# Kernel tuning notes

Hardware: AMD Instinct MI355X
Metric: run time of the kernel (lower is better)

## Reference

```python
import jax, jax.numpy as jnp
import numpy as np

TAU = 0.5
EPS = 1e-12  # F.normalize eps


def _l2_normalize(z):
    n = jnp.linalg.norm(z, axis=1, keepdims=True)
    return z / jnp.maximum(n, EPS)


def _semi_loss(a, b):
    # a, b: [N, d], already raw embeddings; normalize then exp(sim/tau)
    an = _l2_normalize(a)
    bn = _l2_normalize(b)
    refl = jnp.exp(jnp.matmul(an, an.T) / TAU)      # [N, N]
    between = jnp.exp(jnp.matmul(an, bn.T) / TAU)   # [N, N]
    pos = jnp.diagonal(between)
    denom = refl.sum(axis=1) + between.sum(axis=1) - jnp.diagonal(refl)
    return -jnp.log(pos / denom)


def setup_inputs() -> dict:
    key = jax.random.key(0)
    k1, k2 = jax.random.split(key)
    z1 = jax.random.normal(k1, (8192, 256), dtype=jnp.float32)
    z2 = jax.random.normal(k2, (8192, 256), dtype=jnp.float32)
    return {"z1": z1, "z2": z2, "mean": 1}


def reference(z1, z2, mean):
    l1 = _semi_loss(z1, z2)
    l2 = _semi_loss(z2, z1)
    ret = (l1 + l2) * 0.5
    return ret.mean() if mean else ret.sum()
```

## Files before the change

### kernel.cpp

```cpp
#include <hip/hip_runtime.h>
#include <hip/hip_bf16.h>
#include <hip/hip_fp8.h>

#define N_ROWS 8192
#define NZ 16384
#define DIM 256
#define TAU_INV 2.0f
#define BT 128
#define AT 64
#define NTILE 128
#define NCHUNK 16
#define SEGT 4
#define NSEG 4224
#define PSTRIDE 768

typedef float f32x4 __attribute__((ext_vector_type(4)));
typedef long lx2 __attribute__((ext_vector_type(2)));

__global__ __launch_bounds__(256) void normalize_kernel(
    const float* __restrict__ z1, const float* __restrict__ z2,
    unsigned char* __restrict__ Z8, float* __restrict__ pos)
{
    const int tid = threadIdx.x;
    const int wave = tid >> 6;
    const int lane = tid & 63;
    const int row = blockIdx.x * 4 + wave;

    const float4 a = ((const float4*)(z1 + (size_t)row * DIM))[lane];
    const float4 b = ((const float4*)(z2 + (size_t)row * DIM))[lane];

    auto wsum = [&](float v) -> float {
        #pragma unroll
        for (int m = 1; m < 64; m <<= 1) v += __shfl_xor(v, m, 64);
        return v;
    };

    const float na2 = wsum(a.x*a.x + a.y*a.y + a.z*a.z + a.w*a.w);
    const float nb2 = wsum(b.x*b.x + b.y*b.y + b.z*b.z + b.w*b.w);
    const float sa = 16.0f / sqrtf(na2);
    const float sb = 16.0f / sqrtf(nb2);

    const float av[4] = {a.x*sa, a.y*sa, a.z*sa, a.w*sa};
    const float bv[4] = {b.x*sb, b.y*sb, b.z*sb, b.w*sb};
    unsigned char pa[4], pb[4];
    float qd = 0.0f;
    #pragma unroll
    for (int k = 0; k < 4; ++k) {
        __hip_fp8_e4m3 qa(av[k]);
        __hip_fp8_e4m3 qb(bv[k]);
        pa[k] = qa.__x; pb[k] = qb.__x;
        qd += float(qa) * float(qb);
    }
    const int g  = (lane >> 1) & 7;
    const int pp = ((g & 3) << 1) | (g >> 2);
    const int off = (lane >> 4) * 64 + pp * 8 + (lane & 1) * 4;
    *(uchar4*)(Z8 + (size_t)row * DIM + off) = *(uchar4*)pa;
    *(uchar4*)(Z8 + (size_t)(N_ROWS + row) * DIM + off) = *(uchar4*)pb;

    qd = wsum(qd);
    if (lane == 0) pos[row] = qd * 0.00390625f;
}

#define MFMA8(A, B, C) __builtin_amdgcn_mfma_f32_16x16x32_fp8_fp8(A, B, C, 0, 0, 0)

#define STAGE(TF, KH, SL)                                                      \
  { const unsigned char* gsrc = pb0 + (size_t)(TF) * 32768 + (KH) * 128;       \
    _Pragma("unroll")                                                          \
    for (int c = 0; c < 4; ++c)                                                \
      __builtin_amdgcn_global_load_lds(                                        \
        (const __attribute__((address_space(1))) void*)(gsrc + c * 2048),      \
        (__attribute__((address_space(3))) void*)(Ls + wvLds + (SL)*4096 + c*1024), \
        16, 0, 0); }

#define MFMA_HALF(KH)                                                          \
  __builtin_amdgcn_s_setprio(1);                                               \
  _Pragma("unroll")                                                            \
  for (int fr = 0; fr < 4; ++fr) {                                             \
    acc[fr][0] = MFMA8(aR[KH][0][fr].x, b00.x, acc[fr][0]);                    \
    acc[fr][0] = MFMA8(aR[KH][0][fr].y, b00.y, acc[fr][0]);                    \
    acc[fr][1] = MFMA8(aR[KH][0][fr].x, b10.x, acc[fr][1]);                    \
    acc[fr][1] = MFMA8(aR[KH][0][fr].y, b10.y, acc[fr][1]);                    \
  }                                                                            \
  _Pragma("unroll")                                                            \
  for (int fr = 0; fr < 4; ++fr) {                                             \
    acc[fr][0] = MFMA8(aR[KH][1][fr].x, b01.x, acc[fr][0]);                    \
    acc[fr][0] = MFMA8(aR[KH][1][fr].y, b01.y, acc[fr][0]);                    \
    acc[fr][1] = MFMA8(aR[KH][1][fr].x, b11.x, acc[fr][1]);                    \
    acc[fr][1] = MFMA8(aR[KH][1][fr].y, b11.y, acc[fr][1]);                    \
  }

#define PHASE(KH, SLOT, NW, DOISS, TF2, KH2, SLOT2)                            \
  {                                                                            \
    if (DOISS) STAGE(TF2, KH2, SLOT2);                                         \
    asm volatile("s_waitcnt vmcnt(" #NW ")" ::: "memory");                     \
    lx2 b00, b10, b01, b11;                                                    \
    asm volatile("ds_read_b128 %0, %1" : "=v"(b00) : "v"(bA00 + (SLOT)*4096)); \
    asm volatile("ds_read_b128 %0, %1" : "=v"(b10) : "v"(bA10 + (SLOT)*4096)); \
    asm volatile("ds_read_b128 %0, %1" : "=v"(b01) : "v"(bA01 + (SLOT)*4096)); \
    asm volatile("ds_read_b128 %0, %1" : "=v"(b11) : "v"(bA11 + (SLOT)*4096)); \
    asm volatile("s_waitcnt lgkmcnt(0)" ::: "memory");                         \
    __builtin_amdgcn_sched_barrier(0);                                         \
    MFMA_HALF(KH)                                                              \
    __builtin_amdgcn_s_setprio(0);                                             \
  }

#define EPILOG(T)                                                              \
  if ((T) < nt) {                                                              \
    _Pragma("unroll")                                                          \
    for (int fr = 0; fr < 4; ++fr)                                             \
      _Pragma("unroll")                                                        \
      for (int fc = 0; fc < 2; ++fc)                                           \
        _Pragma("unroll")                                                      \
        for (int r = 0; r < 4; ++r)                                            \
          acc[fr][fc][r] = exp2f(acc[fr][fc][r] * SC);                         \
    if ((T) == 0 && s4 == 0) {                                                 \
      const int add = (ri & 1) << 6;                                           \
      _Pragma("unroll")                                                        \
      for (int fr = 0; fr < 4; ++fr) {                                         \
        const int gi = fr * 16 + lq * 4;                                       \
        _Pragma("unroll")                                                      \
        for (int fc = 0; fc < 2; ++fc) {                                       \
          const int cj = wv * 32 + fc * 16 + lm;                               \
          _Pragma("unroll")                                                    \
          for (int r = 0; r < 4; ++r)                                          \
            if (cj <= gi + r + add) acc[fr][fc][r] = 0.0f;                     \
        }                                                                      \
      }                                                                        \
    }                                                                          \
    _Pragma("unroll")                                                          \
    for (int fr = 0; fr < 4; ++fr)                                             \
      _Pragma("unroll")                                                        \
      for (int r = 0; r < 4; ++r)                                              \
        rowacc[fr][r] += acc[fr][0][r] + acc[fr][1][r];                        \
    _Pragma("unroll")                                                          \
    for (int fc = 0; fc < 2; ++fc) {                                           \
      float s_ = 0.0f;                                                         \
      _Pragma("unroll")                                                        \
      for (int fr = 0; fr < 4; ++fr)                                           \
        _Pragma("unroll")                                                      \
        for (int r = 0; r < 4; ++r) s_ += acc[fr][fc][r];                      \
      colacc[T][fc] = s_;                                                      \
    }                                                                          \
  }

template <bool TWO_STAGE>
__global__ __launch_bounds__(256, 3) void gram_kernel(
    const unsigned char* __restrict__ Z,
    float* __restrict__ part, float* __restrict__ S)
{
    const int sid = (blockIdx.x & 7) * (NSEG / 8) + (blockIdx.x >> 3);
    int g = (int)((260.0f - sqrtf(67600.0f - 16.0f * (float)sid)) * 0.125f);
    g = g < 0 ? 0 : (g > 31 ? 31 : g);
    while (260 * g - 4 * g * g > sid) --g;
    while (g < 31 && 260 * (g + 1) - 4 * (g + 1) * (g + 1) <= sid) ++g;
    const int local = sid - (260 * g - 4 * g * g);
    const int v  = 32 - g;
    const int r8i = local / v;
    const int s4 = local - r8i * v;
    const int ri = 8 * g + r8i;
    const int tj0 = (ri >> 1) + SEGT * s4;
    const int nt = (NTILE - tj0 < SEGT) ? (NTILE - tj0) : SEGT;
    const int tf1 = nt > 1 ? 1 : 0;
    const int tf2 = nt > 2 ? 2 : tf1;
    const int tf3 = nt > 3 ? 3 : tf2;

    __shared__ unsigned char Ls[49152];

    const int tid  = threadIdx.x;
    const int wv   = tid >> 6;
    const int lane = tid & 63;
    const int lm = lane & 15, lq = lane >> 4;
    const unsigned wvLds = wv * 12288;

    lx2 aR[2][2][4];
    {
        const unsigned char* pa = Z + (size_t)(ri * AT + lm) * DIM + lq * 16;
        #pragma unroll
        for (int fr = 0; fr < 4; ++fr)
            #pragma unroll
            for (int kh = 0; kh < 2; ++kh)
                #pragma unroll
                for (int s = 0; s < 2; ++s)
                    aR[kh][s][fr] =
                        *(const lx2*)(pa + fr * 4096 + kh * 128 + s * 64);
    }

    const int l8 = lane >> 3;
    const int g7 = lane & 7;
    const unsigned char* pb0 =
        Z + (size_t)(tj0 * BT + wv * 32 + l8) * DIM + ((g7 ^ l8) << 4);

    const unsigned ldsBase = (unsigned)(unsigned long long)
        (__attribute__((address_space(3))) unsigned char*)Ls;
    const unsigned wvB = ldsBase + wvLds + (unsigned)(lm * 128);
    const unsigned q0 = (unsigned)(((lq    ) ^ (lm & 7)) << 4);
    const unsigned q1 = (unsigned)(((lq + 4) ^ (lm & 7)) << 4);
    const unsigned bA00 = wvB + q0;
    const unsigned bA01 = wvB + q1;
    const unsigned bA10 = wvB + 2048 + q0;
    const unsigned bA11 = wvB + 2048 + q1;

    const float SC = 2.8853900817779268f / 256.0f;

    f32x4 rowacc[4] = {};
    float colacc[4][2] = {};

    STAGE(0, 0, 0)
    STAGE(0, 1, 1)

    { f32x4 acc[4][2] = {};
      PHASE(0, 0, 8, 1, tf1, 0, 2)
      PHASE(1, 1, 8, 1, tf1, 1, 0)
      EPILOG(0)
    }
    { f32x4 acc[4][2] = {};
      PHASE(0, 2, 8, 1, tf2, 0, 1)
      PHASE(1, 0, 8, 1, tf2, 1, 2)
      EPILOG(1)
    }
    { f32x4 acc[4][2] = {};
      PHASE(0, 1, 8, 1, tf3, 0, 0)
      PHASE(1, 2, 8, 1, tf3, 1, 1)
      EPILOG(2)
    }
    { f32x4 acc[4][2] = {};
      PHASE(0, 0, 4, 0, 0, 0, 0)
      PHASE(1, 1, 0, 0, 0, 0, 0)
      EPILOG(3)
    }

    #pragma unroll
    for (int t = 0; t < 4; ++t)
        #pragma unroll
        for (int fc = 0; fc < 2; ++fc) {
            float s = colacc[t][fc];
            s += __shfl_xor(s, 16, 64);
            s += __shfl_xor(s, 32, 64);
            if (lq == 0) {
                const int cj = wv * 32 + fc * 16 + lm;
                if (TWO_STAGE)
                    part[(size_t)sid * PSTRIDE + 256 + t * 128 + cj] = s;
                else if (t < nt)
                    atomicAdd(&S[(tj0 + t) * BT + cj], s);
            }
        }

    float* dstr = TWO_STAGE ? (part + (size_t)sid * PSTRIDE) : nullptr;
    #pragma unroll
    for (int fr = 0; fr < 4; ++fr) {
        f32x4 rs;
        #pragma unroll
        for (int r = 0; r < 4; ++r) {
            float s = rowacc[fr][r];
            s += __shfl_xor(s, 1, 64);
            s += __shfl_xor(s, 2, 64);
            s += __shfl_xor(s, 4, 64);
            s += __shfl_xor(s, 8, 64);
            rs[r] = s;
        }
        if (lm == 0) {
            const int rr = fr * 16 + lq * 4;
            if (TWO_STAGE) *(f32x4*)(dstr + wv * 64 + rr) = rs;
            else {
                #pragma unroll
                for (int r = 0; r < 4; ++r)
                    atomicAdd(&S[ri * AT + rr + r], rs[r]);
            }
        }
    }
}

__global__ __launch_bounds__(256) void reduce_kernel(
    const float* __restrict__ part, float* __restrict__ S2,
    float* __restrict__ out)
{
    const int chunk = blockIdx.y;
    const int tid = threadIdx.x;
    const int r = blockIdx.x * 256 + tid;
    const int ri = r >> 6, rr = r & 63;
    const int gg = ri >> 3;
    const int nseg = 32 - gg;
    const int sid0 = 260 * gg - 4 * gg * gg + (ri & 7) * nseg;
    const int tj = r >> 7, cc = r & 127;
    const int nr = 2 * tj + 2;
    const int T = 4 * nseg + nr;

    if (chunk == 0 && r == 0) out[0] = 0.0f;

    float s = 0.0f;
    for (int m = chunk; m < T; m += NCHUNK) {
        size_t addr;
        if (m < 4 * nseg) {
            addr = (size_t)(sid0 + (m >> 2)) * PSTRIDE + (m & 3) * 64 + rr;
        } else {
            const int rip = m - 4 * nseg;
            const int dtj = tj - (rip >> 1);
            const int gp = rip >> 3;
            const int sidc = 260 * gp - 4 * gp * gp + (rip & 7) * (32 - gp)
                           + (dtj >> 2);
            addr = (size_t)sidc * PSTRIDE + 256 + (dtj & 3) * 128 + cc;
        }
        s += part[addr];
    }
    S2[(size_t)chunk * NZ + r] = s;
}

__global__ __launch_bounds__(256) void loss2_kernel(
    const float* __restrict__ S2, const float* __restrict__ pos,
    float* __restrict__ out)
{
    const int i = blockIdx.x * 256 + threadIdx.x;
    float den1 = 0.0f, den2 = 0.0f;
    #pragma unroll
    for (int c = 0; c < NCHUNK; ++c) {
        den1 += S2[(size_t)c * NZ + i];
        den2 += S2[(size_t)c * NZ + N_ROWS + i];
    }
    float v = 0.5f * (logf(den1) + logf(den2)) - TAU_INV * pos[i];

    __shared__ float red[4];
    #pragma unroll
    for (int m = 1; m < 64; m <<= 1) v += __shfl_xor(v, m, 64);
    if ((threadIdx.x & 63) == 0) red[threadIdx.x >> 6] = v;
    __syncthreads();
    if (threadIdx.x == 0)
        atomicAdd(out, (red[0] + red[1] + red[2] + red[3]) * (1.0f / N_ROWS));
}

__global__ __launch_bounds__(256) void loss_kernel(
    const float* __restrict__ S, const float* __restrict__ pos,
    float* __restrict__ out)
{
    const int i = blockIdx.x * 256 + threadIdx.x;
    float v = 0.5f * (logf(S[i]) + logf(S[N_ROWS + i])) - TAU_INV * pos[i];

    __shared__ float red[4];
    #pragma unroll
    for (int m = 1; m < 64; m <<= 1) v += __shfl_xor(v, m, 64);
    if ((threadIdx.x & 63) == 0) red[threadIdx.x >> 6] = v;
    __syncthreads();
    if (threadIdx.x == 0)
        atomicAdd(out, (red[0] + red[1] + red[2] + red[3]) * (1.0f / N_ROWS));
}

extern "C" void kernel_launch(void* const* d_in, const int* in_sizes, int n_in,
                              void* d_out, int out_size, void* d_ws, size_t ws_size,
                              hipStream_t stream)
{
    const float* z1 = (const float*)d_in[0];
    const float* z2 = (const float*)d_in[1];
    float* out = (float*)d_out;

    char* ws = (char*)d_ws;
    unsigned char* Z8 = (unsigned char*)ws;
    float* pos  = (float*)(ws + 4194304);
    float* S2   = (float*)(ws + 4227072);
    float* part = (float*)(ws + 5275648);
    const size_t need = 5275648 + (size_t)NSEG * PSTRIDE * 4;

    normalize_kernel<<<N_ROWS / 4, 256, 0, stream>>>(z1, z2, Z8, pos);

    if (ws_size >= need) {
        gram_kernel<true><<<NSEG, 256, 0, stream>>>(Z8, part, nullptr);
        dim3 rg(NZ / 256, NCHUNK);
        reduce_kernel<<<rg, 256, 0, stream>>>(part, S2, out);
        loss2_kernel<<<N_ROWS / 256, 256, 0, stream>>>(S2, pos, out);
    } else {
        hipMemsetAsync(S2, 0, NZ * sizeof(float), stream);
        hipMemsetAsync(out, 0, sizeof(float), stream);
        gram_kernel<false><<<NSEG, 256, 0, stream>>>(Z8, nullptr, S2);
        loss_kernel<<<N_ROWS / 256, 256, 0, stream>>>(S2, pos, out);
    }
}
```

Before: 160.6 us.

## Share B tiles across waves via common LDS with 2x2 wave grid

Replaces the per-wave private B staging (each wave loading its own 32 columns) with a shared LDS buffer that all four waves fill cooperatively, and reorganizes the 64x128 tile so waves form a 2x2 grid (32 rows x 64 columns each). Each wave now holds fewer A fragments in registers and reads four B fragments per k-step. Block barriers are added before each phase, and the partial-sum layout and reduction indexing are updated to handle the extra row/column partials. The change aims at better operand reuse and fewer registers, at the cost of block-wide synchronization and larger partial buffers.

```diff
diff --git a/kernel.cpp b/kernel.cpp
--- a/kernel.cpp
+++ b/kernel.cpp
@@ -12,7 +12,7 @@
 #define NCHUNK 16
 #define SEGT 4
 #define NSEG 4224
-#define PSTRIDE 768
+#define PSTRIDE 1152
 
 typedef float f32x4 __attribute__((ext_vector_type(4)));
 typedef long lx2 __attribute__((ext_vector_type(2)));
@@ -64,63 +64,73 @@
 #define MFMA8(A, B, C) __builtin_amdgcn_mfma_f32_16x16x32_fp8_fp8(A, B, C, 0, 0, 0)
 
 #define STAGE(TF, KH, SL)                                                      \
-  { const unsigned char* gsrc = pb0 + (size_t)(TF) * 32768 + (KH) * 128;       \
+  { const unsigned char* gsrc = pbSt + (size_t)(TF) * 32768 + (KH) * 128;      \
     _Pragma("unroll")                                                          \
     for (int c = 0; c < 4; ++c)                                                \
       __builtin_amdgcn_global_load_lds(                                        \
         (const __attribute__((address_space(1))) void*)(gsrc + c * 2048),      \
-        (__attribute__((address_space(3))) void*)(Ls + wvLds + (SL)*4096 + c*1024), \
+        (__attribute__((address_space(3))) void*)(Ls + (SL) * 16384 + (wv * 4 + c) * 1024), \
         16, 0, 0); }
 
-#define MFMA_HALF(KH)                                                          \
-  __builtin_amdgcn_s_setprio(1);                                               \
-  _Pragma("unroll")                                                            \
-  for (int fr = 0; fr < 4; ++fr) {                                             \
-    acc[fr][0] = MFMA8(aR[KH][0][fr].x, b00.x, acc[fr][0]);                    \
-    acc[fr][0] = MFMA8(aR[KH][0][fr].y, b00.y, acc[fr][0]);                    \
-    acc[fr][1] = MFMA8(aR[KH][0][fr].x, b10.x, acc[fr][1]);                    \
-    acc[fr][1] = MFMA8(aR[KH][0][fr].y, b10.y, acc[fr][1]);                    \
-  }                                                                            \
-  _Pragma("unroll")                                                            \
-  for (int fr = 0; fr < 4; ++fr) {                                             \
-    acc[fr][0] = MFMA8(aR[KH][1][fr].x, b01.x, acc[fr][0]);                    \
-    acc[fr][0] = MFMA8(aR[KH][1][fr].y, b01.y, acc[fr][0]);                    \
-    acc[fr][1] = MFMA8(aR[KH][1][fr].x, b11.x, acc[fr][1]);                    \
-    acc[fr][1] = MFMA8(aR[KH][1][fr].y, b11.y, acc[fr][1]);                    \
-  }
-
-#define PHASE(KH, SLOT, NW, DOISS, TF2, KH2, SLOT2)                            \
+#define DSR(DST, ADDR, SOFF)                                                   \
+  asm volatile("ds_read_b128 %0, %1 offset:" SOFF : "=v"(DST) : "v"(ADDR));
+
+#define PHASE(KH, SOFF, VMW, DOST, TF2, KH2, SL2)                              \
   {                                                                            \
-    if (DOISS) STAGE(TF2, KH2, SLOT2);                                         \
-    asm volatile("s_waitcnt vmcnt(" #NW ")" ::: "memory");                     \
-    lx2 b00, b10, b01, b11;                                                    \
-    asm volatile("ds_read_b128 %0, %1" : "=v"(b00) : "v"(bA00 + (SLOT)*4096)); \
-    asm volatile("ds_read_b128 %0, %1" : "=v"(b10) : "v"(bA10 + (SLOT)*4096)); \
-    asm volatile("ds_read_b128 %0, %1" : "=v"(b01) : "v"(bA01 + (SLOT)*4096)); \
-    asm volatile("ds_read_b128 %0, %1" : "=v"(b11) : "v"(bA11 + (SLOT)*4096)); \
+    asm volatile("s_waitcnt vmcnt(" VMW ") lgkmcnt(0)\n\ts_barrier" ::: "memory"); \
+    if (DOST) STAGE(TF2, KH2, SL2)                                             \
+    lx2 b00, b01, b02, b03, b10, b11, b12, b13;                                \
+    DSR(b00, bR0, SOFF) DSR(b01, bR1, SOFF)                                    \
+    DSR(b02, bR2, SOFF) DSR(b03, bR3, SOFF)                                    \
+    DSR(b10, bS0, SOFF) DSR(b11, bS1, SOFF)                                    \
+    DSR(b12, bS2, SOFF) DSR(b13, bS3, SOFF)                                    \
+    asm volatile("s_waitcnt lgkmcnt(4)" ::: "memory");                         \
+    __builtin_amdgcn_sched_barrier(0);                                         \
+    __builtin_amdgcn_s_setprio(1);                                             \
+    _Pragma("unroll")                                                          \
+    for (int fr = 0; fr < 2; ++fr) {                                           \
+      acc[fr][0] = MFMA8(aR[KH][0][fr].x, b00.x, acc[fr][0]);                  \
+      acc[fr][0] = MFMA8(aR[KH][0][fr].y, b00.y, acc[fr][0]);                  \
+      acc[fr][1] = MFMA8(aR[KH][0][fr].x, b01.x, acc[fr][1]);                  \
+      acc[fr][1] = MFMA8(aR[KH][0][fr].y, b01.y, acc[fr][1]);                  \
+      acc[fr][2] = MFMA8(aR[KH][0][fr].x, b02.x, acc[fr][2]);                  \
+      acc[fr][2] = MFMA8(aR[KH][0][fr].y, b02.y, acc[fr][2]);                  \
+      acc[fr][3] = MFMA8(aR[KH][0][fr].x, b03.x, acc[fr][3]);                  \
+      acc[fr][3] = MFMA8(aR[KH][0][fr].y, b03.y, acc[fr][3]);                  \
+    }                                                                          \
     asm volatile("s_waitcnt lgkmcnt(0)" ::: "memory");                         \
     __builtin_amdgcn_sched_barrier(0);                                         \
-    MFMA_HALF(KH)                                                              \
+    _Pragma("unroll")                                                          \
+    for (int fr = 0; fr < 2; ++fr) {                                           \
+      acc[fr][0] = MFMA8(aR[KH][1][fr].x, b10.x, acc[fr][0]);                  \
+      acc[fr][0] = MFMA8(aR[KH][1][fr].y, b10.y, acc[fr][0]);                  \
+      acc[fr][1] = MFMA8(aR[KH][1][fr].x, b11.x, acc[fr][1]);                  \
+      acc[fr][1] = MFMA8(aR[KH][1][fr].y, b11.y, acc[fr][1]);                  \
+      acc[fr][2] = MFMA8(aR[KH][1][fr].x, b12.x, acc[fr][2]);                  \
+      acc[fr][2] = MFMA8(aR[KH][1][fr].y, b12.y, acc[fr][2]);                  \
+      acc[fr][3] = MFMA8(aR[KH][1][fr].x, b13.x, acc[fr][3]);                  \
+      acc[fr][3] = MFMA8(aR[KH][1][fr].y, b13.y, acc[fr][3]);                  \
+    }                                                                          \
     __builtin_amdgcn_s_setprio(0);                                             \
   }
 
 #define EPILOG(T)                                                              \
   if ((T) < nt) {                                                              \
     _Pragma("unroll")                                                          \
-    for (int fr = 0; fr < 4; ++fr)                                             \
+    for (int fr = 0; fr < 2; ++fr)                                             \
       _Pragma("unroll")                                                        \
-      for (int fc = 0; fc < 2; ++fc)                                           \
+      for (int fc = 0; fc < 4; ++fc)                                           \
         _Pragma("unroll")                                                      \
         for (int r = 0; r < 4; ++r)                                            \
           acc[fr][fc][r] = exp2f(acc[fr][fc][r] * SC);                         \
     if ((T) == 0 && s4 == 0) {                                                 \
       const int add = (ri & 1) << 6;                                           \
       _Pragma("unroll")                                                        \
-      for (int fr = 0; fr < 4; ++fr) {                                         \
-        const int gi = fr * 16 + lq * 4;                                       \
+      for (int fr = 0; fr < 2; ++fr) {                                         \
+        const int gi = wr * 32 + fr * 16 + lq * 4;                             \
         _Pragma("unroll")                                                      \
-        for (int fc = 0; fc < 2; ++fc) {                                       \
-          const int cj = wv * 32 + fc * 16 + lm;                               \
+        for (int fc = 0; fc < 4; ++fc) {                                       \
+          const int cj = wc * 64 + fc * 16 + lm;                               \
           _Pragma("unroll")                                                    \
           for (int r = 0; r < 4; ++r)                                          \
             if (cj <= gi + r + add) acc[fr][fc][r] = 0.0f;                     \
@@ -128,15 +138,16 @@
       }                                                                        \
     }                                                                          \
     _Pragma("unroll")                                                          \
-    for (int fr = 0; fr < 4; ++fr)                                             \
+    for (int fr = 0; fr < 2; ++fr)                                             \
       _Pragma("unroll")                                                        \
       for (int r = 0; r < 4; ++r)                                              \
-        rowacc[fr][r] += acc[fr][0][r] + acc[fr][1][r];                        \
-    _Pragma("unroll")                                                          \
-    for (int fc = 0; fc < 2; ++fc) {                                           \
+        rowacc[fr][r] += acc[fr][0][r] + acc[fr][1][r]                         \
+                       + acc[fr][2][r] + acc[fr][3][r];                        \
+    _Pragma("unroll")                                                          \
+    for (int fc = 0; fc < 4; ++fc) {                                           \
       float s_ = 0.0f;                                                         \
       _Pragma("unroll")                                                        \
-      for (int fr = 0; fr < 4; ++fr)                                           \
+      for (int fr = 0; fr < 2; ++fr)                                           \
         _Pragma("unroll")                                                      \
         for (int r = 0; r < 4; ++r) s_ += acc[fr][fc][r];                      \
       colacc[T][fc] = s_;                                                      \
@@ -169,14 +180,15 @@
     const int tid  = threadIdx.x;
     const int wv   = tid >> 6;
     const int lane = tid & 63;
+    const int wr = wv >> 1, wc = wv & 1;
     const int lm = lane & 15, lq = lane >> 4;
-    const unsigned wvLds = wv * 12288;
-
-    lx2 aR[2][2][4];
+
+    lx2 aR[2][2][2];
     {
-        const unsigned char* pa = Z + (size_t)(ri * AT + lm) * DIM + lq * 16;
+        const unsigned char* pa =
+            Z + (size_t)(ri * AT + wr * 32 + lm) * DIM + lq * 16;
         #pragma unroll
-        for (int fr = 0; fr < 4; ++fr)
+        for (int fr = 0; fr < 2; ++fr)
             #pragma unroll
             for (int kh = 0; kh < 2; ++kh)
                 #pragma unroll
@@ -187,67 +199,67 @@
 
     const int l8 = lane >> 3;
     const int g7 = lane & 7;
-    const unsigned char* pb0 =
+    const unsigned char* pbSt =
         Z + (size_t)(tj0 * BT + wv * 32 + l8) * DIM + ((g7 ^ l8) << 4);
 
     const unsigned ldsBase = (unsigned)(unsigned long long)
         (__attribute__((address_space(3))) unsigned char*)Ls;
-    const unsigned wvB = ldsBase + wvLds + (unsigned)(lm * 128);
+    const unsigned rdB = ldsBase + (unsigned)((wc * 64 + lm) * 128);
     const unsigned q0 = (unsigned)(((lq    ) ^ (lm & 7)) << 4);
     const unsigned q1 = (unsigned)(((lq + 4) ^ (lm & 7)) << 4);
-    const unsigned bA00 = wvB + q0;
-    const unsigned bA01 = wvB + q1;
-    const unsigned bA10 = wvB + 2048 + q0;
-    const unsigned bA11 = wvB + 2048 + q1;
+    const unsigned bR0 = rdB + q0,        bS0 = rdB + q1;
+    const unsigned bR1 = rdB + 2048 + q0, bS1 = rdB + 2048 + q1;
+    const unsigned bR2 = rdB + 4096 + q0, bS2 = rdB + 4096 + q1;
+    const unsigned bR3 = rdB + 6144 + q0, bS3 = rdB + 6144 + q1;
 
     const float SC = 2.8853900817779268f / 256.0f;
 
-    f32x4 rowacc[4] = {};
-    float colacc[4][2] = {};
+    f32x4 rowacc[2] = {};
+    float colacc[4][4] = {};
 
     STAGE(0, 0, 0)
     STAGE(0, 1, 1)
 
-    { f32x4 acc[4][2] = {};
-      PHASE(0, 0, 8, 1, tf1, 0, 2)
-      PHASE(1, 1, 8, 1, tf1, 1, 0)
+    { f32x4 acc[2][4] = {};
+      PHASE(0, "0",     "4", 1, tf1, 0, 2)
+      PHASE(1, "16384", "4", 1, tf1, 1, 0)
       EPILOG(0)
     }
-    { f32x4 acc[4][2] = {};
-      PHASE(0, 2, 8, 1, tf2, 0, 1)
-      PHASE(1, 0, 8, 1, tf2, 1, 2)
+    { f32x4 acc[2][4] = {};
+      PHASE(0, "32768", "4", 1, tf2, 0, 1)
+      PHASE(1, "0",     "4", 1, tf2, 1, 2)
       EPILOG(1)
     }
-    { f32x4 acc[4][2] = {};
-      PHASE(0, 1, 8, 1, tf3, 0, 0)
-      PHASE(1, 2, 8, 1, tf3, 1, 1)
+    { f32x4 acc[2][4] = {};
+      PHASE(0, "16384", "4", 1, tf3, 0, 0)
+      PHASE(1, "32768", "4", 1, tf3, 1, 1)
       EPILOG(2)
     }
-    { f32x4 acc[4][2] = {};
-      PHASE(0, 0, 4, 0, 0, 0, 0)
-      PHASE(1, 1, 0, 0, 0, 0, 0)
+    { f32x4 acc[2][4] = {};
+      PHASE(0, "0",     "4", 0, 0, 0, 0)
+      PHASE(1, "16384", "0", 0, 0, 0, 0)
       EPILOG(3)
     }
 
     #pragma unroll
     for (int t = 0; t < 4; ++t)
         #pragma unroll
-        for (int fc = 0; fc < 2; ++fc) {
+        for (int fc = 0; fc < 4; ++fc) {
             float s = colacc[t][fc];
             s += __shfl_xor(s, 16, 64);
             s += __shfl_xor(s, 32, 64);
             if (lq == 0) {
-                const int cj = wv * 32 + fc * 16 + lm;
+                const int cc = wc * 64 + fc * 16 + lm;
                 if (TWO_STAGE)
-                    part[(size_t)sid * PSTRIDE + 256 + t * 128 + cj] = s;
+                    part[(size_t)sid * PSTRIDE + 128 + t * 256 + wr * 128 + cc] = s;
                 else if (t < nt)
-                    atomicAdd(&S[(tj0 + t) * BT + cj], s);
+                    atomicAdd(&S[(tj0 + t) * BT + cc], s);
             }
         }
 
     float* dstr = TWO_STAGE ? (part + (size_t)sid * PSTRIDE) : nullptr;
     #pragma unroll
-    for (int fr = 0; fr < 4; ++fr) {
+    for (int fr = 0; fr < 2; ++fr) {
         f32x4 rs;
         #pragma unroll
         for (int r = 0; r < 4; ++r) {
@@ -259,8 +271,8 @@
             rs[r] = s;
         }
         if (lm == 0) {
-            const int rr = fr * 16 + lq * 4;
-            if (TWO_STAGE) *(f32x4*)(dstr + wv * 64 + rr) = rs;
+            const int rr = wr * 32 + fr * 16 + lq * 4;
+            if (TWO_STAGE) *(f32x4*)(dstr + wc * 64 + rr) = rs;
             else {
                 #pragma unroll
                 for (int r = 0; r < 4; ++r)
@@ -283,22 +295,24 @@
     const int sid0 = 260 * gg - 4 * gg * gg + (ri & 7) * nseg;
     const int tj = r >> 7, cc = r & 127;
     const int nr = 2 * tj + 2;
-    const int T = 4 * nseg + nr;
+    const int T = 2 * nseg + 2 * nr;
 
     if (chunk == 0 && r == 0) out[0] = 0.0f;
 
     float s = 0.0f;
     for (int m = chunk; m < T; m += NCHUNK) {
         size_t addr;
-        if (m < 4 * nseg) {
-            addr = (size_t)(sid0 + (m >> 2)) * PSTRIDE + (m & 3) * 64 + rr;
+        if (m < 2 * nseg) {
+            addr = (size_t)(sid0 + (m >> 1)) * PSTRIDE + (m & 1) * 64 + rr;
         } else {
-            const int rip = m - 4 * nseg;
+            const int m2 = m - 2 * nseg;
+            const int rip = m2 >> 1;
             const int dtj = tj - (rip >> 1);
             const int gp = rip >> 3;
             const int sidc = 260 * gp - 4 * gp * gp + (rip & 7) * (32 - gp)
                            + (dtj >> 2);
-            addr = (size_t)sidc * PSTRIDE + 256 + (dtj & 3) * 128 + cc;
+            addr = (size_t)sidc * PSTRIDE + 128 + (dtj & 3) * 256
+                 + (m2 & 1) * 128 + cc;
         }
         s += part[addr];
     }
```

Result: no change. 163.6 us (+1.9%).
